# Optimization experiments

Hardware: AMD Instinct MI355X
Metric: run time of the kernel (lower is better)

## Reference

```python
import jax, jax.numpy as jnp
import numpy as np

BASE_ALPHA = 0.1
NUM_ITER = 4


def setup_inputs() -> dict:
    key = jax.random.key(0)
    k1, k2 = jax.random.split(key)
    pred = jax.random.normal(k1, (8, 8192, 3), dtype=jnp.float32)
    partial = jax.random.normal(k2, (8, 2048, 3), dtype=jnp.float32)
    return {"pred": pred, "partial": partial}


def _pairwise_dist(x, y):
    x2 = jnp.sum(x * x, axis=-1)[..., :, None]          # [B, N, 1]
    y2 = jnp.sum(y * y, axis=-1)[..., None, :]          # [B, 1, M]
    xy = jnp.einsum('bnd,bmd->bnm', x, y)               # [B, N, M]
    return jnp.sqrt(jnp.maximum(x2 + y2 - 2.0 * xy, 0.0))


def reference(pred, partial):
    refined = pred
    for _ in range(NUM_ITER):
        dist = _pairwise_dist(refined, partial)          # [B, N, M]
        min_dist = jnp.min(dist, axis=-1)                # [B, N]
        min_idx = jnp.argmin(dist, axis=-1)              # [B, N]
        nearest = jnp.take_along_axis(partial, min_idx[..., None], axis=1)  # [B, N, 3]
        dist_norm = min_dist / (jnp.max(min_dist, axis=-1, keepdims=True) + 1e-6)
        alpha = BASE_ALPHA * (2.0 - dist_norm)           # [B, N]
        refined = refined + alpha[..., None] * (nearest - refined)
    return refined
```

## Files before the change

### kernel.cpp

```cpp
#include <hip/hip_runtime.h>

#define B 8
#define N 8192
#define M 2048
#define NITER 4
#define BASE_ALPHA 0.1f

#define NTHR 1024
#define NPT 32
#define NSPLIT 32
#define JS (M / NSPLIT)
#define JQ (JS / 4)
#define PT 8
#define PPB (NPT * PT)
#define NBLK (B * N / PPB)
#define BPB (NBLK / B)

#define OFF_AUX   (1024 * 1024)
#define OFF_SLOTS (1536 * 1024)


typedef float f2 __attribute__((ext_vector_type(2)));

__device__ __forceinline__ unsigned int ord32(float t) {
    unsigned int u = __float_as_uint(t);
    return u ^ ((unsigned int)((int)u >> 31) | 0x80000000u);
}
__device__ __forceinline__ float dec32(unsigned int h) {
    return __uint_as_float((h & 0x80000000u) ? (h ^ 0x80000000u) : ~h);
}

__global__ __launch_bounds__(NTHR, 4) void iter_kernel(const float* __restrict__ pred,
                                                       const float* __restrict__ partial,
                                                       float4* __restrict__ pos4,
                                                       uint2* __restrict__ aux,
                                                       float* __restrict__ slots,
                                                       int iter) {
    __shared__ float4 sX[M / 4], sY[M / 4], sZ[M / 4], sW[M / 4];
    __shared__ unsigned long long lkeys[16][PPB];
    __shared__ float4 lpos[PPB];
    __shared__ float redbuf[4];
    __shared__ float mxsh;

    const int tid = threadIdx.x;
    const int b = blockIdx.x >> 5;
    const int blk = blockIdx.x & 31;
    const int gp0 = b * N + blk * PPB;

    const float* pa = partial + b * M * 3;
    if (tid < M / 4) {
        int sp = tid & 31, jq = tid >> 5;
        const float* p0 = pa + (sp * JS + jq * 4) * 3;
        float a0 = p0[0], a1 = p0[1],  a2 = p0[2];
        float b0 = p0[3], b1 = p0[4],  b2 = p0[5];
        float c0 = p0[6], c1 = p0[7],  c2 = p0[8];
        float d0 = p0[9], d1 = p0[10], d2 = p0[11];
        sX[tid] = make_float4(-2.f * a0, -2.f * b0, -2.f * c0, -2.f * d0);
        sY[tid] = make_float4(-2.f * a1, -2.f * b1, -2.f * c1, -2.f * d1);
        sZ[tid] = make_float4(-2.f * a2, -2.f * b2, -2.f * c2, -2.f * d2);
        sW[tid] = make_float4(a0 * a0 + a1 * a1 + a2 * a2, b0 * b0 + b1 * b1 + b2 * b2,
                              c0 * c0 + c1 * c1 + c2 * c2, d0 * d0 + d1 * d1 + d2 * d2);
    }
    if (iter > 0 && tid < 64) {
        float v = slots[b * BPB + (tid & 31)];
        #pragma unroll
        for (int o = 16; o > 0; o >>= 1) v = fmaxf(v, __shfl_xor(v, o));
        if (tid == 0) mxsh = v;
    }
    __syncthreads();

    if (tid < PPB) {
        const int p = gp0 + tid;
        float rx, ry, rz;
        if (iter == 0) {
            const float* pp = pred + (unsigned long long)p * 3;
            rx = pp[0]; ry = pp[1]; rz = pp[2];
        } else {
            float4 f = pos4[p];
            uint2 a = aux[p];
            float md = __uint_as_float(a.x);
            int lg = (int)a.y;
            int bs = lg >> 6, bj = lg & 63;
            int i4 = ((bj >> 2) * 32 + bs) * 4 + (bj & 3);
            float ny0 = -0.5f * ((const float*)sX)[i4];
            float ny1 = -0.5f * ((const float*)sY)[i4];
            float ny2 = -0.5f * ((const float*)sZ)[i4];
            float inv = 1.0f / (mxsh + 1e-6f);
            float alpha = BASE_ALPHA * (2.0f - md * inv);
            rx = fmaf(alpha, ny0 - f.x, f.x);
            ry = fmaf(alpha, ny1 - f.y, f.y);
            rz = fmaf(alpha, ny2 - f.z, f.z);
        }
        float w = rx * rx + ry * ry + rz * rz;
        lpos[tid] = make_float4(rx, ry, rz, w);
        pos4[p] = make_float4(rx, ry, rz, w);
    }
    __syncthreads();

    const int split = tid >> 5;
    const int pt = tid & 31;
    const int wave = tid >> 6;

    f2 sx[PT], sy[PT], sz[PT];
    #pragma unroll
    for (int k = 0; k < PT; ++k) {
        float4 r = lpos[pt + k * NPT];
        sx[k] = (f2){r.x, r.x}; sy[k] = (f2){r.y, r.y}; sz[k] = (f2){r.z, r.z};
    }
    f2 acc[PT];
    #pragma unroll
    for (int k = 0; k < PT; ++k) acc[k] = (f2){3.402823466e+38f, 3.402823466e+38f};

    #pragma unroll 2
    for (int jq = 0; jq < JQ; ++jq) {
        float4 qx = sX[jq * 32 + split], qy = sY[jq * 32 + split];
        float4 qz = sZ[jq * 32 + split], qw = sW[jq * 32 + split];
        f2 qx01 = (f2){qx.x, qx.y}, qx23 = (f2){qx.z, qx.w};
        f2 qy01 = (f2){qy.x, qy.y}, qy23 = (f2){qy.z, qy.w};
        f2 qz01 = (f2){qz.x, qz.y}, qz23 = (f2){qz.z, qz.w};
        f2 qw01 = (f2){qw.x, qw.y}, qw23 = (f2){qw.z, qw.w};
        #pragma unroll
        for (int k = 0; k < PT; ++k) {
            f2 t01 = __builtin_elementwise_fma(sx[k], qx01,
                     __builtin_elementwise_fma(sy[k], qy01,
                     __builtin_elementwise_fma(sz[k], qz01, qw01)));
            f2 t23 = __builtin_elementwise_fma(sx[k], qx23,
                     __builtin_elementwise_fma(sy[k], qy23,
                     __builtin_elementwise_fma(sz[k], qz23, qw23)));
            acc[k] = __builtin_elementwise_min(acc[k],
                     __builtin_elementwise_min(t01, t23));
        }
    }

    #pragma unroll
    for (int k = 0; k < PT; ++k) {
        float vbk = fminf(acc[k].x, acc[k].y);
        unsigned int hi = ord32(vbk);
        unsigned int lo = (unsigned int)split;
        unsigned int ohi = __shfl_xor(hi, 32), olo = __shfl_xor(lo, 32);
        if (ohi < hi || (ohi == hi && olo < lo)) { hi = ohi; lo = olo; }
        if ((tid & 32) == 0)
            lkeys[wave][pt + k * NPT] = (((unsigned long long)hi) << 32) | lo;
    }
    __syncthreads();

    if (tid < PPB) {
        unsigned long long best = lkeys[0][tid];
        #pragma unroll
        for (int r = 1; r < 16; ++r) {
            unsigned long long c = lkeys[r][tid];
            if (c < best) best = c;
        }
        const int bsplit = (int)(unsigned int)(best & 0xFFFFFFFFull);
        const float tstar = dec32((unsigned int)(best >> 32));
        const float4 f4 = lpos[tid];
        const float md = sqrtf(fmaxf(f4.w + tstar, 0.0f));

        float bt = 3.402823466e+38f; int bj = 0;
        for (int jq = 0; jq < JQ; ++jq) {
            float4 qx = sX[jq * 32 + bsplit], qy = sY[jq * 32 + bsplit];
            float4 qz = sZ[jq * 32 + bsplit], qw = sW[jq * 32 + bsplit];
            float t0 = fmaf(f4.x, qx.x, fmaf(f4.y, qy.x, fmaf(f4.z, qz.x, qw.x)));
            float t1 = fmaf(f4.x, qx.y, fmaf(f4.y, qy.y, fmaf(f4.z, qz.y, qw.y)));
            float t2 = fmaf(f4.x, qx.z, fmaf(f4.y, qy.z, fmaf(f4.z, qz.z, qw.z)));
            float t3 = fmaf(f4.x, qx.w, fmaf(f4.y, qy.w, fmaf(f4.z, qz.w, qw.w)));
            if (t0 < bt) { bt = t0; bj = jq * 4 + 0; }
            if (t1 < bt) { bt = t1; bj = jq * 4 + 1; }
            if (t2 < bt) { bt = t2; bj = jq * 4 + 2; }
            if (t3 < bt) { bt = t3; bj = jq * 4 + 3; }
        }
        aux[gp0 + tid] = make_uint2(__float_as_uint(md),
                                    (unsigned int)(bsplit * JS + bj));

        float wm = md;
        for (int o = 32; o > 0; o >>= 1) wm = fmaxf(wm, __shfl_down(wm, o));
        if ((tid & 63) == 0) redbuf[tid >> 6] = wm;
    }
    __syncthreads();
    if (tid == 0)
        slots[b * BPB + blk] = fmaxf(fmaxf(redbuf[0], redbuf[1]),
                                     fmaxf(redbuf[2], redbuf[3]));
}

__global__ __launch_bounds__(256) void final_kernel(const float* __restrict__ partial,
                                                    const float4* __restrict__ pos4,
                                                    const uint2* __restrict__ aux,
                                                    const float* __restrict__ slots,
                                                    float* __restrict__ out) {
    __shared__ float mxsh;
    const int p = blockIdx.x * 256 + threadIdx.x;
    const int b = p >> 13;
    if (threadIdx.x < 64) {
        float v = slots[b * BPB + (threadIdx.x & 31)];
        #pragma unroll
        for (int o = 16; o > 0; o >>= 1) v = fmaxf(v, __shfl_xor(v, o));
        if (threadIdx.x == 0) mxsh = v;
    }
    __syncthreads();
    float4 f = pos4[p];
    uint2 a = aux[p];
    float md = __uint_as_float(a.x);
    const float* py = partial + ((unsigned long long)(b * M + (int)a.y)) * 3;
    float y0 = py[0], y1 = py[1], y2 = py[2];
    float inv = 1.0f / (mxsh + 1e-6f);
    float alpha = BASE_ALPHA * (2.0f - md * inv);
    float* po = out + (unsigned long long)p * 3;
    po[0] = fmaf(alpha, y0 - f.x, f.x);
    po[1] = fmaf(alpha, y1 - f.y, f.y);
    po[2] = fmaf(alpha, y2 - f.z, f.z);
}

extern "C" void kernel_launch(void* const* d_in, const int* in_sizes, int n_in,
                              void* d_out, int out_size, void* d_ws, size_t ws_size,
                              hipStream_t stream) {
    const float* pred = (const float*)d_in[0];
    const float* partial = (const float*)d_in[1];
    char* ws = (char*)d_ws;
    float4* pos4 = (float4*)ws;
    uint2* aux = (uint2*)(ws + OFF_AUX);
    float* slots = (float*)(ws + OFF_SLOTS);
    float* out = (float*)d_out;

    for (int it = 0; it < NITER; ++it)
        hipLaunchKernelGGL(iter_kernel, dim3(NBLK), dim3(NTHR), 0, stream,
                           pred, partial, pos4, aux, slots, it);
    hipLaunchKernelGGL(final_kernel, dim3(B * N / 256), dim3(256), 0, stream,
                       partial, pos4, aux, slots, out);
}
```

Measured before the change: 118.6 us.

## Track argmin quad in main loop, store nearest coords, drop block reductions

The main distance loop now records which quad index produced the running minimum, so the second pass only re-evaluates one float4 quad instead of scanning all 64 candidates of the winning split. The nearest point's coordinates are written to a float4 aux buffer, which removes the gather from partial in the next iteration and in the final kernel. Per-wave maxima go straight to double-buffered slots, removing the end-of-block syncthreads reduction, and each consumer reduces 128 slots with shuffles. The partial staging load and the position update run in separate thread groups, which removes one barrier and uses vectorized float4 loads. The per-element index select adds a compare and two selects to the hot loop and raises register pressure.

Measured after the change: 119.7 us, median of 2. No clear change (+0.9%).

```diff
diff --git a/kernel.cpp b/kernel.cpp
--- a/kernel.cpp
+++ b/kernel.cpp
@@ -9,15 +9,16 @@
 #define NTHR 1024
 #define NPT 32
 #define NSPLIT 32
-#define JS (M / NSPLIT)
-#define JQ (JS / 4)
+#define JS 64
+#define JQ 16
 #define PT 8
-#define PPB (NPT * PT)
-#define NBLK (B * N / PPB)
-#define BPB (NBLK / B)
+#define PPB 256
+#define NBLK 256
+#define BPB 32
+#define NSLOT (BPB * 4)
 
 #define OFF_AUX   (1024 * 1024)
-#define OFF_SLOTS (1536 * 1024)
+#define OFF_SLOTS (2 * 1024 * 1024)
 
 
 typedef float f2 __attribute__((ext_vector_type(2)));
@@ -33,43 +34,34 @@
 __global__ __launch_bounds__(NTHR, 4) void iter_kernel(const float* __restrict__ pred,
                                                        const float* __restrict__ partial,
                                                        float4* __restrict__ pos4,
-                                                       uint2* __restrict__ aux,
-                                                       float* __restrict__ slots,
+                                                       float4* __restrict__ aux4,
+                                                       const float* __restrict__ slots_in,
+                                                       float* __restrict__ slots_out,
                                                        int iter) {
     __shared__ float4 sX[M / 4], sY[M / 4], sZ[M / 4], sW[M / 4];
     __shared__ unsigned long long lkeys[16][PPB];
     __shared__ float4 lpos[PPB];
-    __shared__ float redbuf[4];
-    __shared__ float mxsh;
 
     const int tid = threadIdx.x;
     const int b = blockIdx.x >> 5;
     const int blk = blockIdx.x & 31;
     const int gp0 = b * N + blk * PPB;
+    const int wave = tid >> 6;
 
     const float* pa = partial + b * M * 3;
-    if (tid < M / 4) {
-        int sp = tid & 31, jq = tid >> 5;
-        const float* p0 = pa + (sp * JS + jq * 4) * 3;
-        float a0 = p0[0], a1 = p0[1],  a2 = p0[2];
-        float b0 = p0[3], b1 = p0[4],  b2 = p0[5];
-        float c0 = p0[6], c1 = p0[7],  c2 = p0[8];
-        float d0 = p0[9], d1 = p0[10], d2 = p0[11];
-        sX[tid] = make_float4(-2.f * a0, -2.f * b0, -2.f * c0, -2.f * d0);
-        sY[tid] = make_float4(-2.f * a1, -2.f * b1, -2.f * c1, -2.f * d1);
-        sZ[tid] = make_float4(-2.f * a2, -2.f * b2, -2.f * c2, -2.f * d2);
-        sW[tid] = make_float4(a0 * a0 + a1 * a1 + a2 * a2, b0 * b0 + b1 * b1 + b2 * b2,
-                              c0 * c0 + c1 * c1 + c2 * c2, d0 * d0 + d1 * d1 + d2 * d2);
-    }
-    if (iter > 0 && tid < 64) {
-        float v = slots[b * BPB + (tid & 31)];
-        #pragma unroll
-        for (int o = 16; o > 0; o >>= 1) v = fmaxf(v, __shfl_xor(v, o));
-        if (tid == 0) mxsh = v;
-    }
-    __syncthreads();
-
-    if (tid < PPB) {
+    if (tid >= 512) {
+        int u = tid - 512;
+        int sp = u & 31, jq = u >> 5;
+        const float4* src = (const float4*)(pa + (sp * JS + jq * 4) * 3);
+        float4 A = src[0], Bv = src[1], C = src[2];
+        sX[u] = make_float4(-2.f * A.x, -2.f * A.w, -2.f * Bv.z, -2.f * C.y);
+        sY[u] = make_float4(-2.f * A.y, -2.f * Bv.x, -2.f * Bv.w, -2.f * C.z);
+        sZ[u] = make_float4(-2.f * A.z, -2.f * Bv.y, -2.f * C.x, -2.f * C.w);
+        sW[u] = make_float4(A.x * A.x + A.y * A.y + A.z * A.z,
+                            A.w * A.w + Bv.x * Bv.x + Bv.y * Bv.y,
+                            Bv.z * Bv.z + Bv.w * Bv.w + C.x * C.x,
+                            C.y * C.y + C.z * C.z + C.w * C.w);
+    } else if (tid < PPB) {
         const int p = gp0 + tid;
         float rx, ry, rz;
         if (iter == 0) {
@@ -77,19 +69,17 @@
             rx = pp[0]; ry = pp[1]; rz = pp[2];
         } else {
             float4 f = pos4[p];
-            uint2 a = aux[p];
-            float md = __uint_as_float(a.x);
-            int lg = (int)a.y;
-            int bs = lg >> 6, bj = lg & 63;
-            int i4 = ((bj >> 2) * 32 + bs) * 4 + (bj & 3);
-            float ny0 = -0.5f * ((const float*)sX)[i4];
-            float ny1 = -0.5f * ((const float*)sY)[i4];
-            float ny2 = -0.5f * ((const float*)sZ)[i4];
-            float inv = 1.0f / (mxsh + 1e-6f);
-            float alpha = BASE_ALPHA * (2.0f - md * inv);
-            rx = fmaf(alpha, ny0 - f.x, f.x);
-            ry = fmaf(alpha, ny1 - f.y, f.y);
-            rz = fmaf(alpha, ny2 - f.z, f.z);
+            float4 a = aux4[p];
+            int lane = tid & 63;
+            float2 sv = ((const float2*)(slots_in + b * NSLOT))[lane];
+            float wm = fmaxf(sv.x, sv.y);
+            #pragma unroll
+            for (int o = 32; o > 0; o >>= 1) wm = fmaxf(wm, __shfl_xor(wm, o));
+            float inv = 1.0f / (wm + 1e-6f);
+            float alpha = BASE_ALPHA * (2.0f - a.x * inv);
+            rx = fmaf(alpha, a.y - f.x, f.x);
+            ry = fmaf(alpha, a.z - f.y, f.y);
+            rz = fmaf(alpha, a.w - f.z, f.z);
         }
         float w = rx * rx + ry * ry + rz * rz;
         lpos[tid] = make_float4(rx, ry, rz, w);
@@ -99,7 +89,6 @@
 
     const int split = tid >> 5;
     const int pt = tid & 31;
-    const int wave = tid >> 6;
 
     f2 sx[PT], sy[PT], sz[PT];
     #pragma unroll
@@ -107,11 +96,11 @@
         float4 r = lpos[pt + k * NPT];
         sx[k] = (f2){r.x, r.x}; sy[k] = (f2){r.y, r.y}; sz[k] = (f2){r.z, r.z};
     }
-    f2 acc[PT];
-    #pragma unroll
-    for (int k = 0; k < PT; ++k) acc[k] = (f2){3.402823466e+38f, 3.402823466e+38f};
-
-    #pragma unroll 2
+    float acc[PT]; int idq[PT];
+    #pragma unroll
+    for (int k = 0; k < PT; ++k) { acc[k] = 3.402823466e+38f; idq[k] = 0; }
+
+    #pragma unroll 4
     for (int jq = 0; jq < JQ; ++jq) {
         float4 qx = sX[jq * 32 + split], qy = sY[jq * 32 + split];
         float4 qz = sZ[jq * 32 + split], qw = sW[jq * 32 + split];
@@ -127,16 +116,18 @@
             f2 t23 = __builtin_elementwise_fma(sx[k], qx23,
                      __builtin_elementwise_fma(sy[k], qy23,
                      __builtin_elementwise_fma(sz[k], qz23, qw23)));
-            acc[k] = __builtin_elementwise_min(acc[k],
-                     __builtin_elementwise_min(t01, t23));
+            f2 m2 = __builtin_elementwise_min(t01, t23);
+            float h = fminf(m2.x, m2.y);
+            bool lt = h < acc[k];
+            acc[k] = lt ? h : acc[k];
+            idq[k] = lt ? jq : idq[k];
         }
     }
 
     #pragma unroll
     for (int k = 0; k < PT; ++k) {
-        float vbk = fminf(acc[k].x, acc[k].y);
-        unsigned int hi = ord32(vbk);
-        unsigned int lo = (unsigned int)split;
+        unsigned int hi = ord32(acc[k]);
+        unsigned int lo = (unsigned int)(split * JQ + idq[k]);
         unsigned int ohi = __shfl_xor(hi, 32), olo = __shfl_xor(lo, 32);
         if (ohi < hi || (ohi == hi && olo < lo)) { hi = ohi; lo = olo; }
         if ((tid & 32) == 0)
@@ -151,63 +142,51 @@
             unsigned long long c = lkeys[r][tid];
             if (c < best) best = c;
         }
-        const int bsplit = (int)(unsigned int)(best & 0xFFFFFFFFull);
+        const unsigned int code = (unsigned int)(best & 0xFFFFFFFFull);
+        const int bsplit = (int)(code >> 4), bjq = (int)(code & 15);
         const float tstar = dec32((unsigned int)(best >> 32));
         const float4 f4 = lpos[tid];
         const float md = sqrtf(fmaxf(f4.w + tstar, 0.0f));
 
-        float bt = 3.402823466e+38f; int bj = 0;
-        for (int jq = 0; jq < JQ; ++jq) {
-            float4 qx = sX[jq * 32 + bsplit], qy = sY[jq * 32 + bsplit];
-            float4 qz = sZ[jq * 32 + bsplit], qw = sW[jq * 32 + bsplit];
-            float t0 = fmaf(f4.x, qx.x, fmaf(f4.y, qy.x, fmaf(f4.z, qz.x, qw.x)));
-            float t1 = fmaf(f4.x, qx.y, fmaf(f4.y, qy.y, fmaf(f4.z, qz.y, qw.y)));
-            float t2 = fmaf(f4.x, qx.z, fmaf(f4.y, qy.z, fmaf(f4.z, qz.z, qw.z)));
-            float t3 = fmaf(f4.x, qx.w, fmaf(f4.y, qy.w, fmaf(f4.z, qz.w, qw.w)));
-            if (t0 < bt) { bt = t0; bj = jq * 4 + 0; }
-            if (t1 < bt) { bt = t1; bj = jq * 4 + 1; }
-            if (t2 < bt) { bt = t2; bj = jq * 4 + 2; }
-            if (t3 < bt) { bt = t3; bj = jq * 4 + 3; }
-        }
-        aux[gp0 + tid] = make_uint2(__float_as_uint(md),
-                                    (unsigned int)(bsplit * JS + bj));
+        const int qi = bjq * 32 + bsplit;
+        float4 qx = sX[qi], qy = sY[qi], qz = sZ[qi], qw = sW[qi];
+        float t0 = fmaf(f4.x, qx.x, fmaf(f4.y, qy.x, fmaf(f4.z, qz.x, qw.x)));
+        float t1 = fmaf(f4.x, qx.y, fmaf(f4.y, qy.y, fmaf(f4.z, qz.y, qw.y)));
+        float t2 = fmaf(f4.x, qx.z, fmaf(f4.y, qy.z, fmaf(f4.z, qz.z, qw.z)));
+        float t3 = fmaf(f4.x, qx.w, fmaf(f4.y, qy.w, fmaf(f4.z, qz.w, qw.w)));
+        float bt = t0, y0 = qx.x, y1 = qy.x, y2 = qz.x;
+        if (t1 < bt) { bt = t1; y0 = qx.y; y1 = qy.y; y2 = qz.y; }
+        if (t2 < bt) { bt = t2; y0 = qx.z; y1 = qy.z; y2 = qz.z; }
+        if (t3 < bt) { bt = t3; y0 = qx.w; y1 = qy.w; y2 = qz.w; }
+        aux4[gp0 + tid] = make_float4(md, -0.5f * y0, -0.5f * y1, -0.5f * y2);
 
         float wm = md;
+        #pragma unroll
         for (int o = 32; o > 0; o >>= 1) wm = fmaxf(wm, __shfl_down(wm, o));
-        if ((tid & 63) == 0) redbuf[tid >> 6] = wm;
-    }
-    __syncthreads();
-    if (tid == 0)
-        slots[b * BPB + blk] = fmaxf(fmaxf(redbuf[0], redbuf[1]),
-                                     fmaxf(redbuf[2], redbuf[3]));
-}
-
-__global__ __launch_bounds__(256) void final_kernel(const float* __restrict__ partial,
-                                                    const float4* __restrict__ pos4,
-                                                    const uint2* __restrict__ aux,
-                                                    const float* __restrict__ slots,
+        if ((tid & 63) == 0)
+            slots_out[b * NSLOT + blk * 4 + wave] = wm;
+    }
+}
+
+__global__ __launch_bounds__(256) void final_kernel(const float4* __restrict__ pos4,
+                                                    const float4* __restrict__ aux4,
+                                                    const float* __restrict__ slots_in,
                                                     float* __restrict__ out) {
-    __shared__ float mxsh;
     const int p = blockIdx.x * 256 + threadIdx.x;
     const int b = p >> 13;
-    if (threadIdx.x < 64) {
-        float v = slots[b * BPB + (threadIdx.x & 31)];
-        #pragma unroll
-        for (int o = 16; o > 0; o >>= 1) v = fmaxf(v, __shfl_xor(v, o));
-        if (threadIdx.x == 0) mxsh = v;
-    }
-    __syncthreads();
+    int lane = threadIdx.x & 63;
+    float2 sv = ((const float2*)(slots_in + b * NSLOT))[lane];
+    float wm = fmaxf(sv.x, sv.y);
+    #pragma unroll
+    for (int o = 32; o > 0; o >>= 1) wm = fmaxf(wm, __shfl_xor(wm, o));
     float4 f = pos4[p];
-    uint2 a = aux[p];
-    float md = __uint_as_float(a.x);
-    const float* py = partial + ((unsigned long long)(b * M + (int)a.y)) * 3;
-    float y0 = py[0], y1 = py[1], y2 = py[2];
-    float inv = 1.0f / (mxsh + 1e-6f);
-    float alpha = BASE_ALPHA * (2.0f - md * inv);
+    float4 a = aux4[p];
+    float inv = 1.0f / (wm + 1e-6f);
+    float alpha = BASE_ALPHA * (2.0f - a.x * inv);
     float* po = out + (unsigned long long)p * 3;
-    po[0] = fmaf(alpha, y0 - f.x, f.x);
-    po[1] = fmaf(alpha, y1 - f.y, f.y);
-    po[2] = fmaf(alpha, y2 - f.z, f.z);
+    po[0] = fmaf(alpha, a.y - f.x, f.x);
+    po[1] = fmaf(alpha, a.z - f.y, f.y);
+    po[2] = fmaf(alpha, a.w - f.z, f.z);
 }
 
 extern "C" void kernel_launch(void* const* d_in, const int* in_sizes, int n_in,
@@ -217,13 +196,17 @@
     const float* partial = (const float*)d_in[1];
     char* ws = (char*)d_ws;
     float4* pos4 = (float4*)ws;
-    uint2* aux = (uint2*)(ws + OFF_AUX);
-    float* slots = (float*)(ws + OFF_SLOTS);
+    float4* aux4 = (float4*)(ws + OFF_AUX);
+    float* slots0 = (float*)(ws + OFF_SLOTS);
+    float* slots1 = slots0 + B * NSLOT;
     float* out = (float*)d_out;
 
-    for (int it = 0; it < NITER; ++it)
+    for (int it = 0; it < NITER; ++it) {
+        float* sin  = (it & 1) ? slots0 : slots1;
+        float* sout = (it & 1) ? slots1 : slots0;
         hipLaunchKernelGGL(iter_kernel, dim3(NBLK), dim3(NTHR), 0, stream,
-                           pred, partial, pos4, aux, slots, it);
+                           pred, partial, pos4, aux4, sin, sout, it);
+    }
     hipLaunchKernelGGL(final_kernel, dim3(B * N / 256), dim3(256), 0, stream,
-                       partial, pos4, aux, slots, out);
-}
+                       pos4, aux4, ((NITER - 1) & 1) ? slots1 : slots0, out);
+}
```
